# Kernel optimization log

Hardware: AMD Instinct MI355X
Metric: run time of the kernel (lower is better)

## Reference

```python
import jax, jax.numpy as jnp
import numpy as np

EMBED_DIM = 1024
HEADS = 16
D_HEAD = EMBED_DIM // HEADS
B, S = 4, 2048


def setup_inputs() -> dict:
    key = jax.random.key(0)
    ks = jax.random.split(key, 7)
    scale = 1.0 / np.sqrt(EMBED_DIM)
    inp = {
        "key": jax.random.normal(ks[0], (B, S, EMBED_DIM), jnp.float32),
        "query": jax.random.normal(ks[1], (B, S, EMBED_DIM), jnp.float32),
        "value": jax.random.normal(ks[2], (B, S, EMBED_DIM), jnp.float32),
        # causal boolean mask, broadcastable to [B, H, S, S]
        "mask": jnp.tril(jnp.ones((S, S), dtype=bool))[None, None, :, :] * jnp.ones((B, 1, 1, 1), dtype=bool),
        # nn.Linear weights, stored torch-style as [out_features, in_features]
        "Wq": jax.random.normal(ks[3], (EMBED_DIM, EMBED_DIM), jnp.float32) * scale,
        "Wk": jax.random.normal(ks[4], (EMBED_DIM, EMBED_DIM), jnp.float32) * scale,
        "Wv": jax.random.normal(ks[5], (EMBED_DIM, EMBED_DIM), jnp.float32) * scale,
        "Wo": jax.random.normal(ks[6], (EMBED_DIM, EMBED_DIM), jnp.float32) * scale,
    }
    return inp


def reference(key, query, value, mask, Wq, Wk, Wv, Wo):
    # projections (nn.Linear, bias=False): x @ W.T
    q = query @ Wq.T                                    # [B,S,E]
    k = key @ Wk.T
    v = value @ Wv.T
    # split heads -> [B,H,S,d]
    def split(x):
        return x.reshape(B, S, HEADS, D_HEAD).transpose(0, 2, 1, 3)
    q, k, v = split(q), split(k), split(v)
    # scaled dot-product scores [B,H,S,S]
    scores = jnp.einsum("bhqd,bhkd->bhqk", q, k) / np.sqrt(D_HEAD).astype(np.float32)
    scores = jnp.where(mask, scores, jnp.float32(-1e9))
    attn = jax.nn.softmax(scores, axis=-1)
    # attention output, merge heads
    out = jnp.einsum("bhqk,bhkd->bhqd", attn, v)        # [B,H,S,d]
    out = out.transpose(0, 2, 1, 3).reshape(B, S, EMBED_DIM)
    return out @ Wo.T
```

## Files before the change

kernel.cpp:

```cpp
#include <hip/hip_runtime.h>

#define SEQ 2048
#define EMBED 1024
#define DHEAD 64

typedef _Float16 h8 __attribute__((ext_vector_type(8)));
typedef _Float16 h4 __attribute__((ext_vector_type(4)));
typedef float f4 __attribute__((ext_vector_type(4)));
typedef unsigned int u32;

__device__ __forceinline__ void gload_lds16(const void* g, void* l) {
    __builtin_amdgcn_global_load_lds(
        (const __attribute__((address_space(1))) u32*)g,
        (__attribute__((address_space(3))) u32*)l, 16, 0, 0);
}

__global__ __launch_bounds__(256) void cvt_f16(
    const float* __restrict__ q, const float* __restrict__ k, const float* __restrict__ v,
    const float* __restrict__ wq, const float* __restrict__ wk, const float* __restrict__ wv,
    const float* __restrict__ wo,
    _Float16* __restrict__ q16, _Float16* __restrict__ k16, _Float16* __restrict__ v16,
    _Float16* __restrict__ wq16, _Float16* __restrict__ wk16, _Float16* __restrict__ wv16,
    _Float16* __restrict__ wo16)
{
    int bid = blockIdx.x;
    const float* src;
    _Float16* dst;
    float scale = 1.0f;
    size_t base;
    if (bid < 24576) {
        int seg = bid >> 13;
        base = (size_t)(bid & 8191) * 1024 + threadIdx.x * 4;
        src = seg == 0 ? q : seg == 1 ? k : v;
        dst = seg == 0 ? q16 : seg == 1 ? k16 : v16;
    } else {
        int wb = bid - 24576;
        int seg = wb >> 10;
        base = (size_t)(wb & 1023) * 1024 + threadIdx.x * 4;
        src = seg == 0 ? wq : seg == 1 ? wk : seg == 2 ? wv : wo;
        dst = seg == 0 ? wq16 : seg == 1 ? wk16 : seg == 2 ? wv16 : wo16;
        if (seg == 0) scale = 0.18033688011112042f;
    }
    float4 x = *(const float4*)(src + base);
    h4 y = { (_Float16)(x.x * scale), (_Float16)(x.y * scale),
             (_Float16)(x.z * scale), (_Float16)(x.w * scale) };
    *(h4*)(dst + base) = y;
}

__device__ __forceinline__ void gemm_core(const _Float16* __restrict__ A, const _Float16* __restrict__ W,
                                          int m0, int n0, int tid,
                                          _Float16* As, _Float16* Bs, f4 acc[4][4])
{
    const int lane = tid & 63, wave = tid >> 6;
    const int t16 = lane & 15, quad = lane >> 4;
    const int wm = (wave >> 1) * 64, wn = (wave & 1) * 64;
    const int wb = wave * 64;
    const int u0 = tid, u1 = tid + 256;
    const int r0 = u0 >> 2, c0 = u0 & 3;
    const int r1 = u1 >> 2, c1 = u1 & 3;
    const _Float16* ga0 = A + (size_t)(m0 + r0) * 1024 + c0 * 8;
    const _Float16* ga1 = A + (size_t)(m0 + r1) * 1024 + c1 * 8;
    const _Float16* gb0 = W + (size_t)(n0 + r0) * 1024 + c0 * 8;
    const _Float16* gb1 = W + (size_t)(n0 + r1) * 1024 + c1 * 8;
    _Float16* la0 = As + wb * 8;
    _Float16* la1 = As + (256 + wb) * 8;
    _Float16* lb0 = Bs + wb * 8;
    _Float16* lb1 = Bs + (256 + wb) * 8;

    for (int k0 = 0; k0 < 1024; k0 += 32) {
        __syncthreads();
        gload_lds16(ga0 + k0, la0);
        gload_lds16(ga1 + k0, la1);
        gload_lds16(gb0 + k0, lb0);
        gload_lds16(gb1 + k0, lb1);
        __syncthreads();
        h8 af[4], bf[4];
#pragma unroll
        for (int i = 0; i < 4; ++i)
            af[i] = *(const h8*)(As + (wm + i * 16 + t16) * 32 + quad * 8);
#pragma unroll
        for (int j = 0; j < 4; ++j)
            bf[j] = *(const h8*)(Bs + (wn + j * 16 + t16) * 32 + quad * 8);
#pragma unroll
        for (int i = 0; i < 4; ++i)
#pragma unroll
            for (int j = 0; j < 4; ++j)
                acc[i][j] = __builtin_amdgcn_mfma_f32_16x16x32_f16(af[i], bf[j], acc[i][j], 0, 0, 0);
    }
}

__global__ __launch_bounds__(256) void proj_qkv(
    const _Float16* __restrict__ q16, const _Float16* __restrict__ k16, const _Float16* __restrict__ v16,
    const _Float16* __restrict__ Wq, const _Float16* __restrict__ Wk, const _Float16* __restrict__ Wv,
    _Float16* __restrict__ Qh, _Float16* __restrict__ Kh, _Float16* __restrict__ Vt)
{
    __shared__ _Float16 As[4096], Bs[4096];
    const int tid = threadIdx.x;
    const int z = blockIdx.z;
    const _Float16 *A, *W;
    int m0, n0;
    if (z == 2) { A = Wv; W = v16; m0 = blockIdx.y * 128; n0 = blockIdx.x * 128; }
    else if (z == 0) { A = q16; W = Wq; m0 = blockIdx.x * 128; n0 = blockIdx.y * 128; }
    else { A = k16; W = Wk; m0 = blockIdx.x * 128; n0 = blockIdx.y * 128; }

    f4 acc[4][4];
    const f4 z4 = {0.f, 0.f, 0.f, 0.f};
#pragma unroll
    for (int i = 0; i < 4; ++i)
#pragma unroll
        for (int j = 0; j < 4; ++j) acc[i][j] = z4;

    gemm_core(A, W, m0, n0, tid, As, Bs, acc);

    const int lane = tid & 63, wave = tid >> 6;
    const int t16 = lane & 15, quad = lane >> 4;
    const int wm = (wave >> 1) * 64, wn = (wave & 1) * 64;
#pragma unroll
    for (int i = 0; i < 4; ++i)
#pragma unroll
        for (int j = 0; j < 4; ++j)
#pragma unroll
            for (int reg = 0; reg < 4; ++reg) {
                int gm = m0 + wm + i * 16 + quad * 4 + reg;
                int gn = n0 + wn + j * 16 + t16;
                float vv = acc[i][j][reg];
                if (z < 2) {
                    int b = gm >> 11, s = gm & 2047, h = gn >> 6, dd = gn & 63;
                    _Float16* dst = (z == 0) ? Qh : Kh;
                    dst[(((size_t)(b * 16 + h) * SEQ) + s) * DHEAD + dd] = (_Float16)vv;
                } else {
                    int h = gm >> 6, dd = gm & 63, b = gn >> 11, s = gn & 2047;
                    int jt = s >> 6, ks = s & 63;
                    int j4 = ks >> 4, quadv = (ks >> 2) & 3, regv = ks & 3;
                    int dt = dd >> 4, t16v = dd & 15;
                    size_t off = (size_t)(b * 16 + h) * (SEQ * DHEAD)
                               + (size_t)(jt * 8 + dt * 2 + (j4 >> 1)) * 512
                               + (quadv * 16 + t16v) * 8 + (j4 & 1) * 4 + regv;
                    Vt[off] = (_Float16)vv;
                }
            }
}

__global__ __launch_bounds__(256) void attn3(
    const _Float16* __restrict__ Qh, const _Float16* __restrict__ Kh,
    const _Float16* __restrict__ Vt, _Float16* __restrict__ Ob)
{
    __shared__ _Float16 Kbuf[2][8][512];
    __shared__ _Float16 Vbuf[2][8][512];

    const int tid = threadIdx.x;
    const int lane = tid & 63, wave = tid >> 6;
    const int t16 = lane & 15, quad = lane >> 4;
    const int bh = blockIdx.x;
    const int b = bh >> 4, h = bh & 15;
    const int qb = (gridDim.y - 1) - blockIdx.y;
    const int q0 = qb * 128;
    const int nqt = qb * 2 + 2;

    const _Float16* Qp = Qh + (size_t)bh * SEQ * DHEAD;
    const _Float16* Kp = Kh + (size_t)bh * SEQ * DHEAD;
    const _Float16* Vp = Vt + (size_t)bh * SEQ * DHEAD;

    const int qlo[2] = { q0 + wave * 32, q0 + wave * 32 + 16 };
    const int last0 = (qlo[0] + 15) >> 6;

    h8 qf[2][2];
#pragma unroll
    for (int qb2 = 0; qb2 < 2; ++qb2)
#pragma unroll
        for (int kc = 0; kc < 2; ++kc)
            qf[qb2][kc] = *(const h8*)(Qp + (size_t)(qlo[qb2] + t16) * 64 + kc * 32 + quad * 8);

    const _Float16* Kl = Kp + t16 * 64 + quad * 8;
    const _Float16* Vl = Vp + lane * 8;

#define STAGE(jt_, bufi)                                                                  \
    do {                                                                                  \
        if (wave < 2) {                                                                   \
            _Pragma("unroll")                                                             \
            for (int i_ = 0; i_ < 4; ++i_) {                                              \
                int g_ = wave * 4 + i_;                                                   \
                gload_lds16(Kl + (jt_) * 4096 + (g_ >> 1) * 1024 + (g_ & 1) * 32,         \
                            &Kbuf[bufi][g_][0]);                                          \
            }                                                                             \
        } else {                                                                          \
            _Pragma("unroll")                                                             \
            for (int i_ = 0; i_ < 4; ++i_) {                                              \
                int g_ = (wave - 2) * 4 + i_;                                             \
                gload_lds16(Vl + ((jt_) * 8 + g_) * 512, &Vbuf[bufi][g_][0]);             \
            }                                                                             \
        }                                                                                 \
    } while (0)

    STAGE(0, 0);
    __syncthreads();

    float mv[2] = {-1e30f, -1e30f};
    float lv[2] = {0.f, 0.f};
    f4 o_acc[2][4];
    const f4 z4 = {0.f, 0.f, 0.f, 0.f};
#pragma unroll
    for (int qb2 = 0; qb2 < 2; ++qb2)
#pragma unroll
        for (int dt = 0; dt < 4; ++dt) o_acc[qb2][dt] = z4;

    for (int jt = 0; jt < nqt; ++jt) {
        const int buf = jt & 1;
        if (jt + 1 < nqt) STAGE(jt + 1, buf ^ 1);

        if (jt <= last0) {
            f4 s0[4], s1[4];
#pragma unroll
            for (int j4 = 0; j4 < 4; ++j4) {
                h8 kfa = *(const h8*)(&Kbuf[buf][j4 * 2 + 0][lane * 8]);
                h8 kfb = *(const h8*)(&Kbuf[buf][j4 * 2 + 1][lane * 8]);
                s1[j4] = __builtin_amdgcn_mfma_f32_16x16x32_f16(kfa, qf[1][0], z4, 0, 0, 0);
                s1[j4] = __builtin_amdgcn_mfma_f32_16x16x32_f16(kfb, qf[1][1], s1[j4], 0, 0, 0);
                s0[j4] = __builtin_amdgcn_mfma_f32_16x16x32_f16(kfa, qf[0][0], z4, 0, 0, 0);
                s0[j4] = __builtin_amdgcn_mfma_f32_16x16x32_f16(kfb, qf[0][1], s0[j4], 0, 0, 0);
            }

            h4 pf0[4], pf1[4];
            auto softmax_frag = [&](f4* s, int qb2, h4* pf) {
                const int myq = qlo[qb2] + t16;
                if ((jt << 6) + 63 > qlo[qb2]) {
#pragma unroll
                    for (int j4 = 0; j4 < 4; ++j4)
#pragma unroll
                        for (int reg = 0; reg < 4; ++reg) {
                            int kk = (jt << 6) + j4 * 16 + quad * 4 + reg;
                            if (kk > myq) s[j4][reg] = -1e30f;
                        }
                }
                float mr = s[0][0];
#pragma unroll
                for (int j4 = 0; j4 < 4; ++j4)
#pragma unroll
                    for (int reg = 0; reg < 4; ++reg) mr = fmaxf(mr, s[j4][reg]);
                mr = fmaxf(mr, __shfl_xor(mr, 16, 64));
                mr = fmaxf(mr, __shfl_xor(mr, 32, 64));
                float mn = mv[qb2];
                if (__any(mr > mn + 8.0f)) {
                    mn = fmaxf(mn, mr);
                    float al = __builtin_amdgcn_exp2f(mv[qb2] - mn);
                    mv[qb2] = mn;
                    lv[qb2] *= al;
#pragma unroll
                    for (int dt = 0; dt < 4; ++dt)
#pragma unroll
                        for (int reg = 0; reg < 4; ++reg) o_acc[qb2][dt][reg] *= al;
                }
                float rs = 0.f;
#pragma unroll
                for (int j4 = 0; j4 < 4; ++j4) {
#pragma unroll
                    for (int reg = 0; reg < 4; ++reg) {
                        float p = __builtin_amdgcn_exp2f(s[j4][reg] - mn);
                        s[j4][reg] = p;
                        rs += p;
                    }
                    pf[j4] = (h4){ (_Float16)s[j4][0], (_Float16)s[j4][1],
                                   (_Float16)s[j4][2], (_Float16)s[j4][3] };
                }
                rs += __shfl_xor(rs, 16, 64);
                rs += __shfl_xor(rs, 32, 64);
                lv[qb2] += rs;
            };
            softmax_frag(s0, 0, pf0);
            softmax_frag(s1, 1, pf1);

#pragma unroll
            for (int dt = 0; dt < 4; ++dt) {
#pragma unroll
                for (int j4p = 0; j4p < 2; ++j4p) {
                    h8 v2 = *(const h8*)(&Vbuf[buf][dt * 2 + j4p][lane * 8]);
                    h4 vlo = __builtin_shufflevector(v2, v2, 0, 1, 2, 3);
                    h4 vhi = __builtin_shufflevector(v2, v2, 4, 5, 6, 7);
                    o_acc[0][dt] = __builtin_amdgcn_mfma_f32_16x16x16f16(vlo, pf0[j4p * 2 + 0], o_acc[0][dt], 0, 0, 0);
                    o_acc[0][dt] = __builtin_amdgcn_mfma_f32_16x16x16f16(vhi, pf0[j4p * 2 + 1], o_acc[0][dt], 0, 0, 0);
                    o_acc[1][dt] = __builtin_amdgcn_mfma_f32_16x16x16f16(vlo, pf1[j4p * 2 + 0], o_acc[1][dt], 0, 0, 0);
                    o_acc[1][dt] = __builtin_amdgcn_mfma_f32_16x16x16f16(vhi, pf1[j4p * 2 + 1], o_acc[1][dt], 0, 0, 0);
                }
            }
        }
        __syncthreads();
    }

    _Float16* ep = ((_Float16*)Kbuf) + wave * 1024;
    const int swz = (t16 & 7) << 3;
#pragma unroll
    for (int qb2 = 0; qb2 < 2; ++qb2) {
        float inv = __builtin_amdgcn_rcpf(lv[qb2]);
#pragma unroll
        for (int dt = 0; dt < 4; ++dt) {
            h4 ov = { (_Float16)(o_acc[qb2][dt][0] * inv), (_Float16)(o_acc[qb2][dt][1] * inv),
                      (_Float16)(o_acc[qb2][dt][2] * inv), (_Float16)(o_acc[qb2][dt][3] * inv) };
            *(h4*)(ep + t16 * 64 + ((dt * 16 + quad * 4) ^ swz)) = ov;
        }
        h8 r0 = *(const h8*)(ep + t16 * 64 + ((quad * 8) ^ swz));
        h8 r1 = *(const h8*)(ep + t16 * 64 + ((32 + quad * 8) ^ swz));
        int s = qlo[qb2] + t16;
        _Float16* og = Ob + ((size_t)(b * SEQ + s)) * EMBED + h * DHEAD;
        *(h8*)(og + quad * 8) = r0;
        *(h8*)(og + 32 + quad * 8) = r1;
    }
#undef STAGE
}

__global__ __launch_bounds__(256) void proj_out(
    const _Float16* __restrict__ A, const _Float16* __restrict__ Wo, float* __restrict__ out)
{
    __shared__ _Float16 As[4096], Bs[4096];
    const int tid = threadIdx.x;
    const int m0 = blockIdx.x * 128, n0 = blockIdx.y * 128;
    f4 acc[4][4];
    const f4 z4 = {0.f, 0.f, 0.f, 0.f};
#pragma unroll
    for (int i = 0; i < 4; ++i)
#pragma unroll
        for (int j = 0; j < 4; ++j) acc[i][j] = z4;

    gemm_core(A, Wo, m0, n0, tid, As, Bs, acc);

    const int lane = tid & 63, wave = tid >> 6;
    const int t16 = lane & 15, quad = lane >> 4;
    const int wm = (wave >> 1) * 64, wn = (wave & 1) * 64;
#pragma unroll
    for (int i = 0; i < 4; ++i)
#pragma unroll
        for (int j = 0; j < 4; ++j)
#pragma unroll
            for (int reg = 0; reg < 4; ++reg) {
                int gm = m0 + wm + i * 16 + quad * 4 + reg;
                int gn = n0 + wn + j * 16 + t16;
                out[(size_t)gm * EMBED + gn] = acc[i][j][reg];
            }
}

extern "C" void kernel_launch(void* const* d_in, const int* in_sizes, int n_in,
                              void* d_out, int out_size, void* d_ws, size_t ws_size,
                              hipStream_t stream) {
    const float* key   = (const float*)d_in[0];
    const float* query = (const float*)d_in[1];
    const float* value = (const float*)d_in[2];
    const float* Wq = (const float*)d_in[4];
    const float* Wk = (const float*)d_in[5];
    const float* Wv = (const float*)d_in[6];
    const float* Wo = (const float*)d_in[7];

    char* ws = (char*)d_ws;
    _Float16* v16  = (_Float16*)(ws);
    _Float16* Wq16 = (_Float16*)(ws + (16u << 20));
    _Float16* Wk16 = (_Float16*)(ws + (18u << 20));
    _Float16* Wv16 = (_Float16*)(ws + (20u << 20));
    _Float16* Wo16 = (_Float16*)(ws + (22u << 20));
    _Float16* Qh   = (_Float16*)(ws + (24u << 20));
    _Float16* Kh   = (_Float16*)(ws + (40u << 20));
    _Float16* Vt   = (_Float16*)(ws + (56u << 20));
    _Float16* Ob   = v16;
    _Float16* q16 = (_Float16*)d_out;
    _Float16* k16 = (_Float16*)d_out + 8388608;

    dim3 blk(256);
    cvt_f16<<<dim3(28672), blk, 0, stream>>>(query, key, value, Wq, Wk, Wv, Wo,
                                             q16, k16, v16, Wq16, Wk16, Wv16, Wo16);
    proj_qkv<<<dim3(64, 8, 3), blk, 0, stream>>>(q16, k16, v16, Wq16, Wk16, Wv16, Qh, Kh, Vt);
    attn3<<<dim3(64, 16), blk, 0, stream>>>(Qh, Kh, Vt, Ob);
    proj_out<<<dim3(64, 8), blk, 0, stream>>>(Ob, Wo16, (float*)d_out);
}
```

Before: 347.4 us.

## Pair long and short causal query blocks per workgroup for load balance

Each attention workgroup now processes two query blocks, p and 15-p, one after the other, so every block does the same total number of K/V tiles (34) under the causal mask. The grid shrinks from 64x16 to 64x8 workgroups. This is meant to remove tail imbalance, where blocks near the diagonal finish early and leave compute units idle. In exchange there are fewer workgroups to fill the 256 CUs, more live registers (two sets of Q fragments and accumulators), which may cut occupancy, and the K/V tiles are reloaded for the second block with no sharing.

```diff
diff --git a/kernel.cpp b/kernel.cpp
--- a/kernel.cpp
+++ b/kernel.cpp
@@ -153,23 +153,28 @@
     const int t16 = lane & 15, quad = lane >> 4;
     const int bh = blockIdx.x;
     const int b = bh >> 4, h = bh & 15;
-    const int qb = (gridDim.y - 1) - blockIdx.y;
-    const int q0 = qb * 128;
-    const int nqt = qb * 2 + 2;
+    const int p = blockIdx.y;
+    const int qbA = 15 - p, qbB = p;
+    const int nqtA = 2 * qbA + 2;
+    const int ntot = 34;
 
     const _Float16* Qp = Qh + (size_t)bh * SEQ * DHEAD;
     const _Float16* Kp = Kh + (size_t)bh * SEQ * DHEAD;
     const _Float16* Vp = Vt + (size_t)bh * SEQ * DHEAD;
 
-    const int qlo[2] = { q0 + wave * 32, q0 + wave * 32 + 16 };
-    const int last0 = (qlo[0] + 15) >> 6;
-
-    h8 qf[2][2];
+    const int qloA[2] = { qbA * 128 + wave * 32, qbA * 128 + wave * 32 + 16 };
+    const int qloB[2] = { qbB * 128 + wave * 32, qbB * 128 + wave * 32 + 16 };
+    const int lastA = (qloA[0] + 15) >> 6;
+    const int lastB = (qloB[0] + 15) >> 6;
+
+    h8 qfA[2][2], qfB[2][2];
 #pragma unroll
     for (int qb2 = 0; qb2 < 2; ++qb2)
 #pragma unroll
-        for (int kc = 0; kc < 2; ++kc)
-            qf[qb2][kc] = *(const h8*)(Qp + (size_t)(qlo[qb2] + t16) * 64 + kc * 32 + quad * 8);
+        for (int kc = 0; kc < 2; ++kc) {
+            qfA[qb2][kc] = *(const h8*)(Qp + (size_t)(qloA[qb2] + t16) * 64 + kc * 32 + quad * 8);
+            qfB[qb2][kc] = *(const h8*)(Qp + (size_t)(qloB[qb2] + t16) * 64 + kc * 32 + quad * 8);
+        }
 
     const _Float16* Kl = Kp + t16 * 64 + quad * 8;
     const _Float16* Vl = Vp + lane * 8;
@@ -192,118 +197,129 @@
         }                                                                                 \
     } while (0)
 
+    float mvA[2] = {-1e30f, -1e30f}, lvA[2] = {0.f, 0.f};
+    float mvB[2] = {-1e30f, -1e30f}, lvB[2] = {0.f, 0.f};
+    f4 oA[2][4], oB[2][4];
+    const f4 z4 = {0.f, 0.f, 0.f, 0.f};
+#pragma unroll
+    for (int qb2 = 0; qb2 < 2; ++qb2)
+#pragma unroll
+        for (int dt = 0; dt < 4; ++dt) { oA[qb2][dt] = z4; oB[qb2][dt] = z4; }
+
+    auto tile_step = [&](int jt, int last0, const int* qlo, h8 (&qf)[2][2],
+                         float (&mv)[2], float (&lv)[2], f4 (&o_acc)[2][4], int buf) {
+        if (jt > last0) return;
+        f4 s0[4], s1[4];
+#pragma unroll
+        for (int j4 = 0; j4 < 4; ++j4) {
+            h8 kfa = *(const h8*)(&Kbuf[buf][j4 * 2 + 0][lane * 8]);
+            h8 kfb = *(const h8*)(&Kbuf[buf][j4 * 2 + 1][lane * 8]);
+            s1[j4] = __builtin_amdgcn_mfma_f32_16x16x32_f16(kfa, qf[1][0], z4, 0, 0, 0);
+            s1[j4] = __builtin_amdgcn_mfma_f32_16x16x32_f16(kfb, qf[1][1], s1[j4], 0, 0, 0);
+            s0[j4] = __builtin_amdgcn_mfma_f32_16x16x32_f16(kfa, qf[0][0], z4, 0, 0, 0);
+            s0[j4] = __builtin_amdgcn_mfma_f32_16x16x32_f16(kfb, qf[0][1], s0[j4], 0, 0, 0);
+        }
+
+        h4 pf0[4], pf1[4];
+        auto softmax_frag = [&](f4* s, int qb2, h4* pf) {
+            const int myq = qlo[qb2] + t16;
+            if ((jt << 6) + 63 > qlo[qb2]) {
+#pragma unroll
+                for (int j4 = 0; j4 < 4; ++j4)
+#pragma unroll
+                    for (int reg = 0; reg < 4; ++reg) {
+                        int kk = (jt << 6) + j4 * 16 + quad * 4 + reg;
+                        if (kk > myq) s[j4][reg] = -1e30f;
+                    }
+            }
+            float mr = s[0][0];
+#pragma unroll
+            for (int j4 = 0; j4 < 4; ++j4)
+#pragma unroll
+                for (int reg = 0; reg < 4; ++reg) mr = fmaxf(mr, s[j4][reg]);
+            mr = fmaxf(mr, __shfl_xor(mr, 16, 64));
+            mr = fmaxf(mr, __shfl_xor(mr, 32, 64));
+            float mn = mv[qb2];
+            if (__any(mr > mn + 8.0f)) {
+                mn = fmaxf(mn, mr);
+                float al = __builtin_amdgcn_exp2f(mv[qb2] - mn);
+                mv[qb2] = mn;
+                lv[qb2] *= al;
+#pragma unroll
+                for (int dt = 0; dt < 4; ++dt)
+#pragma unroll
+                    for (int reg = 0; reg < 4; ++reg) o_acc[qb2][dt][reg] *= al;
+            }
+            float rs = 0.f;
+#pragma unroll
+            for (int j4 = 0; j4 < 4; ++j4) {
+#pragma unroll
+                for (int reg = 0; reg < 4; ++reg) {
+                    float ppv = __builtin_amdgcn_exp2f(s[j4][reg] - mn);
+                    s[j4][reg] = ppv;
+                    rs += ppv;
+                }
+                pf[j4] = (h4){ (_Float16)s[j4][0], (_Float16)s[j4][1],
+                               (_Float16)s[j4][2], (_Float16)s[j4][3] };
+            }
+            rs += __shfl_xor(rs, 16, 64);
+            rs += __shfl_xor(rs, 32, 64);
+            lv[qb2] += rs;
+        };
+        softmax_frag(s0, 0, pf0);
+        softmax_frag(s1, 1, pf1);
+
+#pragma unroll
+        for (int dt = 0; dt < 4; ++dt) {
+#pragma unroll
+            for (int j4p = 0; j4p < 2; ++j4p) {
+                h8 v2 = *(const h8*)(&Vbuf[buf][dt * 2 + j4p][lane * 8]);
+                h4 vlo = __builtin_shufflevector(v2, v2, 0, 1, 2, 3);
+                h4 vhi = __builtin_shufflevector(v2, v2, 4, 5, 6, 7);
+                o_acc[0][dt] = __builtin_amdgcn_mfma_f32_16x16x16f16(vlo, pf0[j4p * 2 + 0], o_acc[0][dt], 0, 0, 0);
+                o_acc[0][dt] = __builtin_amdgcn_mfma_f32_16x16x16f16(vhi, pf0[j4p * 2 + 1], o_acc[0][dt], 0, 0, 0);
+                o_acc[1][dt] = __builtin_amdgcn_mfma_f32_16x16x16f16(vlo, pf1[j4p * 2 + 0], o_acc[1][dt], 0, 0, 0);
+                o_acc[1][dt] = __builtin_amdgcn_mfma_f32_16x16x16f16(vhi, pf1[j4p * 2 + 1], o_acc[1][dt], 0, 0, 0);
+            }
+        }
+    };
+
     STAGE(0, 0);
     __syncthreads();
 
-    float mv[2] = {-1e30f, -1e30f};
-    float lv[2] = {0.f, 0.f};
-    f4 o_acc[2][4];
-    const f4 z4 = {0.f, 0.f, 0.f, 0.f};
-#pragma unroll
-    for (int qb2 = 0; qb2 < 2; ++qb2)
-#pragma unroll
-        for (int dt = 0; dt < 4; ++dt) o_acc[qb2][dt] = z4;
-
-    for (int jt = 0; jt < nqt; ++jt) {
-        const int buf = jt & 1;
-        if (jt + 1 < nqt) STAGE(jt + 1, buf ^ 1);
-
-        if (jt <= last0) {
-            f4 s0[4], s1[4];
-#pragma unroll
-            for (int j4 = 0; j4 < 4; ++j4) {
-                h8 kfa = *(const h8*)(&Kbuf[buf][j4 * 2 + 0][lane * 8]);
-                h8 kfb = *(const h8*)(&Kbuf[buf][j4 * 2 + 1][lane * 8]);
-                s1[j4] = __builtin_amdgcn_mfma_f32_16x16x32_f16(kfa, qf[1][0], z4, 0, 0, 0);
-                s1[j4] = __builtin_amdgcn_mfma_f32_16x16x32_f16(kfb, qf[1][1], s1[j4], 0, 0, 0);
-                s0[j4] = __builtin_amdgcn_mfma_f32_16x16x32_f16(kfa, qf[0][0], z4, 0, 0, 0);
-                s0[j4] = __builtin_amdgcn_mfma_f32_16x16x32_f16(kfb, qf[0][1], s0[j4], 0, 0, 0);
-            }
-
-            h4 pf0[4], pf1[4];
-            auto softmax_frag = [&](f4* s, int qb2, h4* pf) {
-                const int myq = qlo[qb2] + t16;
-                if ((jt << 6) + 63 > qlo[qb2]) {
-#pragma unroll
-                    for (int j4 = 0; j4 < 4; ++j4)
-#pragma unroll
-                        for (int reg = 0; reg < 4; ++reg) {
-                            int kk = (jt << 6) + j4 * 16 + quad * 4 + reg;
-                            if (kk > myq) s[j4][reg] = -1e30f;
-                        }
-                }
-                float mr = s[0][0];
-#pragma unroll
-                for (int j4 = 0; j4 < 4; ++j4)
-#pragma unroll
-                    for (int reg = 0; reg < 4; ++reg) mr = fmaxf(mr, s[j4][reg]);
-                mr = fmaxf(mr, __shfl_xor(mr, 16, 64));
-                mr = fmaxf(mr, __shfl_xor(mr, 32, 64));
-                float mn = mv[qb2];
-                if (__any(mr > mn + 8.0f)) {
-                    mn = fmaxf(mn, mr);
-                    float al = __builtin_amdgcn_exp2f(mv[qb2] - mn);
-                    mv[qb2] = mn;
-                    lv[qb2] *= al;
-#pragma unroll
-                    for (int dt = 0; dt < 4; ++dt)
-#pragma unroll
-                        for (int reg = 0; reg < 4; ++reg) o_acc[qb2][dt][reg] *= al;
-                }
-                float rs = 0.f;
-#pragma unroll
-                for (int j4 = 0; j4 < 4; ++j4) {
-#pragma unroll
-                    for (int reg = 0; reg < 4; ++reg) {
-                        float p = __builtin_amdgcn_exp2f(s[j4][reg] - mn);
-                        s[j4][reg] = p;
-                        rs += p;
-                    }
-                    pf[j4] = (h4){ (_Float16)s[j4][0], (_Float16)s[j4][1],
-                                   (_Float16)s[j4][2], (_Float16)s[j4][3] };
-                }
-                rs += __shfl_xor(rs, 16, 64);
-                rs += __shfl_xor(rs, 32, 64);
-                lv[qb2] += rs;
-            };
-            softmax_frag(s0, 0, pf0);
-            softmax_frag(s1, 1, pf1);
-
-#pragma unroll
-            for (int dt = 0; dt < 4; ++dt) {
-#pragma unroll
-                for (int j4p = 0; j4p < 2; ++j4p) {
-                    h8 v2 = *(const h8*)(&Vbuf[buf][dt * 2 + j4p][lane * 8]);
-                    h4 vlo = __builtin_shufflevector(v2, v2, 0, 1, 2, 3);
-                    h4 vhi = __builtin_shufflevector(v2, v2, 4, 5, 6, 7);
-                    o_acc[0][dt] = __builtin_amdgcn_mfma_f32_16x16x16f16(vlo, pf0[j4p * 2 + 0], o_acc[0][dt], 0, 0, 0);
-                    o_acc[0][dt] = __builtin_amdgcn_mfma_f32_16x16x16f16(vhi, pf0[j4p * 2 + 1], o_acc[0][dt], 0, 0, 0);
-                    o_acc[1][dt] = __builtin_amdgcn_mfma_f32_16x16x16f16(vlo, pf1[j4p * 2 + 0], o_acc[1][dt], 0, 0, 0);
-                    o_acc[1][dt] = __builtin_amdgcn_mfma_f32_16x16x16f16(vhi, pf1[j4p * 2 + 1], o_acc[1][dt], 0, 0, 0);
-                }
-            }
-        }
+    for (int t = 0; t < ntot; ++t) {
+        const int buf = t & 1;
+        if (t + 1 < ntot) {
+            int njt = (t + 1 < nqtA) ? (t + 1) : (t + 1 - nqtA);
+            STAGE(njt, buf ^ 1);
+        }
+        if (t < nqtA) tile_step(t, lastA, qloA, qfA, mvA, lvA, oA, buf);
+        else          tile_step(t - nqtA, lastB, qloB, qfB, mvB, lvB, oB, buf);
         __syncthreads();
     }
 
     _Float16* ep = ((_Float16*)Kbuf) + wave * 1024;
     const int swz = (t16 & 7) << 3;
-#pragma unroll
-    for (int qb2 = 0; qb2 < 2; ++qb2) {
-        float inv = __builtin_amdgcn_rcpf(lv[qb2]);
-#pragma unroll
-        for (int dt = 0; dt < 4; ++dt) {
-            h4 ov = { (_Float16)(o_acc[qb2][dt][0] * inv), (_Float16)(o_acc[qb2][dt][1] * inv),
-                      (_Float16)(o_acc[qb2][dt][2] * inv), (_Float16)(o_acc[qb2][dt][3] * inv) };
-            *(h4*)(ep + t16 * 64 + ((dt * 16 + quad * 4) ^ swz)) = ov;
-        }
-        h8 r0 = *(const h8*)(ep + t16 * 64 + ((quad * 8) ^ swz));
-        h8 r1 = *(const h8*)(ep + t16 * 64 + ((32 + quad * 8) ^ swz));
-        int s = qlo[qb2] + t16;
-        _Float16* og = Ob + ((size_t)(b * SEQ + s)) * EMBED + h * DHEAD;
-        *(h8*)(og + quad * 8) = r0;
-        *(h8*)(og + 32 + quad * 8) = r1;
-    }
+    auto epilogue = [&](const int* qlo, float (&lv)[2], f4 (&o_acc)[2][4]) {
+#pragma unroll
+        for (int qb2 = 0; qb2 < 2; ++qb2) {
+            float inv = __builtin_amdgcn_rcpf(lv[qb2]);
+#pragma unroll
+            for (int dt = 0; dt < 4; ++dt) {
+                h4 ov = { (_Float16)(o_acc[qb2][dt][0] * inv), (_Float16)(o_acc[qb2][dt][1] * inv),
+                          (_Float16)(o_acc[qb2][dt][2] * inv), (_Float16)(o_acc[qb2][dt][3] * inv) };
+                *(h4*)(ep + t16 * 64 + ((dt * 16 + quad * 4) ^ swz)) = ov;
+            }
+            h8 r0 = *(const h8*)(ep + t16 * 64 + ((quad * 8) ^ swz));
+            h8 r1 = *(const h8*)(ep + t16 * 64 + ((32 + quad * 8) ^ swz));
+            int s = qlo[qb2] + t16;
+            _Float16* og = Ob + ((size_t)(b * SEQ + s)) * EMBED + h * DHEAD;
+            *(h8*)(og + quad * 8) = r0;
+            *(h8*)(og + 32 + quad * 8) = r1;
+        }
+    };
+    epilogue(qloA, lvA, oA);
+    epilogue(qloB, lvB, oB);
 #undef STAGE
 }
 
@@ -365,6 +381,6 @@
     cvt_f16<<<dim3(28672), blk, 0, stream>>>(query, key, value, Wq, Wk, Wv, Wo,
                                              q16, k16, v16, Wq16, Wk16, Wv16, Wo16);
     proj_qkv<<<dim3(64, 8, 3), blk, 0, stream>>>(q16, k16, v16, Wq16, Wk16, Wv16, Qh, Kh, Vt);
-    attn3<<<dim3(64, 16), blk, 0, stream>>>(Qh, Kh, Vt, Ob);
+    attn3<<<dim3(64, 8), blk, 0, stream>>>(Qh, Kh, Vt, Ob);
     proj_out<<<dim3(64, 8), blk, 0, stream>>>(Ob, Wo16, (float*)d_out);
 }
```

Result: slower. 392.5 us (+13.0%).
